# Kernel optimization log

Hardware: AMD Instinct MI355X
Metric: run time of the kernel (lower is better)

The kernel has to match this reference:

```python
import jax, jax.numpy as jnp
import numpy as np

B, S, D = 2, 2048, 1024
H = 16
HD = D // H  # 64


def setup_inputs() -> dict:
    key = jax.random.key(0)
    k1, k2, k3, k4, k5, k6 = jax.random.split(key, 6)
    hidden_states = jax.random.normal(k1, (B, S, D), dtype=jnp.float32)
    attention_mask = jax.random.randint(k2, (B, S), 0, 2, dtype=jnp.int32)
    scale = 1.0 / np.sqrt(D)
    Wq = jax.random.normal(k3, (D, D), dtype=jnp.float32) * scale
    bq = jax.random.normal(k4, (D,), dtype=jnp.float32) * 0.02
    Wk = jax.random.normal(k5, (D, D), dtype=jnp.float32) * scale
    bk = jax.random.normal(k6, (D,), dtype=jnp.float32) * 0.02
    return {"hidden_states": hidden_states, "attention_mask": attention_mask,
            "Wq": Wq, "bq": bq, "Wk": Wk, "bk": bk}


def _split_heads(x):
    # [B, S, D] -> [B, H, S, HD]
    b, s, _ = x.shape
    return x.reshape(b, s, H, HD).transpose(0, 2, 1, 3)


def reference(hidden_states, attention_mask, Wq, bq, Wk, bk):
    dh = jnp.sqrt(jnp.float32(HD))
    q = _split_heads(hidden_states @ Wq + bq)            # [B,H,S,HD]
    k = _split_heads(hidden_states @ Wk + bk)            # [B,H,S,HD]
    v = q + k                                            # value = Q + K
    k_t = -jax.nn.log_sigmoid(-k)                        # negate the logsigmoid(-K) transform
    scores = jnp.einsum('bhqd,bhkd->bhqk', q, k_t) / dh  # [B,H,S,S]
    # mask applied on the QUERY axis (dim 2), broadcast over key axis (faithful to source)
    mask = (attention_mask[:, None, :, None] == 0)       # [B,1,S,1]
    scores = jnp.where(mask, jnp.float32(-10000.0), scores)
    probs = jax.nn.softmax(scores, axis=-1)              # dropout: eval mode (identity)
    ctx = jnp.einsum('bhqk,bhkd->bhqd', probs, v)        # [B,H,S,HD]
    ctx = ctx.transpose(0, 2, 1, 3).reshape(B, S, D)
    return ctx
```

## Files before the change

### kernel.cpp

```cpp
#include <hip/hip_runtime.h>
#include <hip/hip_bf16.h>

#define B_ 2
#define S_ 2048
#define D_ 1024
#define H_ 16
#define HD_ 64

typedef __attribute__((ext_vector_type(8))) short short8;
typedef __attribute__((ext_vector_type(4))) short short4v;
typedef __attribute__((ext_vector_type(4))) float float4v;

typedef const __attribute__((address_space(1))) void* gas_ptr;
typedef __attribute__((address_space(3))) void* las_ptr;

static __device__ inline void gl_lds16(const void* g, void* l) {
  __builtin_amdgcn_global_load_lds((gas_ptr)g, (las_ptr)l, 16, 0, 0);
}

static __device__ inline float b2f(__hip_bfloat16 h) { return __bfloat162float(h); }

static __device__ inline short f2bs(float x) {
  __hip_bfloat16 h = __float2bfloat16(x);
  union { __hip_bfloat16 h; short s; } u; u.h = h; return u.s;
}
static __device__ inline float bs2f(short s) {
  union { short s; __hip_bfloat16 h; } u; u.s = s; return __bfloat162float(u.h);
}
static __device__ inline short4v pk4(float a, float b, float c, float d) {
  union { __hip_bfloat162 h[2]; short4v s; } u;
  u.h[0] = __float22bfloat162_rn(float2{a, b});
  u.h[1] = __float22bfloat162_rn(float2{c, d});
  return u.s;
}

static __device__ inline float4v mfma32(short8 a, short8 b, float4v c) {
  return __builtin_amdgcn_mfma_f32_16x16x32_bf16(a, b, c, 0, 0, 0);
}
static __device__ inline float4v mfma16(short4v a, short4v b, float4v c) {
  return __builtin_amdgcn_mfma_f32_16x16x16bf16_1k(a, b, c, 0, 0, 0);
}

__global__ __launch_bounds__(256) void pre(
    const float* __restrict__ Wq, const float* __restrict__ Wk,
    const float* __restrict__ hs,
    __hip_bfloat16* __restrict__ Wqt, __hip_bfloat16* __restrict__ Wkt,
    __hip_bfloat16* __restrict__ hsb) {
  if (blockIdx.z == 2) {
    const int blk = blockIdx.y * 16 + blockIdx.x;
    for (int it = 0; it < 8; ++it) {
      const size_t i = (size_t)blk * 16384 + it * 2048 + threadIdx.x * 8;
      const float4v v0 = *(const float4v*)(hs + i);
      const float4v v1 = *(const float4v*)(hs + i + 4);
      short8 s;
      for (int j = 0; j < 4; ++j) { s[j] = f2bs(v0[j]); s[4 + j] = f2bs(v1[j]); }
      *(short8*)(hsb + i) = s;
    }
    return;
  }
  const float* W = blockIdx.z ? Wk : Wq;
  __hip_bfloat16* Wt = blockIdx.z ? Wkt : Wqt;
  __shared__ float t[64][65];
  const int n0 = blockIdx.x * 64, k0 = blockIdx.y * 64;
  const int c = threadIdx.x & 63, r0 = threadIdx.x >> 6;
  for (int i = 0; i < 16; ++i) {
    const int r = i * 4 + r0;
    t[c][r] = W[(size_t)(k0 + r) * D_ + n0 + c];
  }
  __syncthreads();
  for (int i = 0; i < 16; ++i) {
    const int rr = i * 4 + r0;
    Wt[(size_t)(n0 + rr) * D_ + k0 + c] = __float2bfloat16(t[rr][c]);
  }
}

__global__ __launch_bounds__(256) void gemm_fused(
    const __hip_bfloat16* __restrict__ A,
    const __hip_bfloat16* __restrict__ Wqt, const __hip_bfloat16* __restrict__ Wkt,
    const float* __restrict__ bq, const float* __restrict__ bk,
    __hip_bfloat16* __restrict__ q_out, __hip_bfloat16* __restrict__ kt_out,
    __hip_bfloat16* __restrict__ vT) {
  const int n0 = blockIdx.x * 128, m0 = blockIdx.y * 64;
  __shared__ __hip_bfloat16 As[2][64 * 32];
  __shared__ __hip_bfloat16 Bq[2][128 * 32];
  __shared__ __hip_bfloat16 Bk[2][128 * 32];
  const int tid = threadIdx.x, wid = tid >> 6, lane = tid & 63;
  const int wm = (wid >> 1) * 32, wn = (wid & 1) * 64;
  const int l15 = lane & 15, l4 = lane >> 4;
  const float4v zz = {0.f, 0.f, 0.f, 0.f};
  float4v accq[2][4], acck[2][4];
  for (int i = 0; i < 2; ++i)
    for (int j = 0; j < 4; ++j) { accq[i][j] = zz; acck[i][j] = zz; }
  const int arow = wid * 16 + (lane >> 2);
  const int brow = wid * 32 + (lane >> 2);
  const int lk8 = (lane & 3) * 8;
  gl_lds16(A + (size_t)(m0 + arow) * D_ + lk8, As[0] + wid * 512);
  gl_lds16(Wqt + (size_t)(n0 + brow) * D_ + lk8, Bq[0] + wid * 1024);
  gl_lds16(Wqt + (size_t)(n0 + brow + 16) * D_ + lk8, Bq[0] + wid * 1024 + 512);
  gl_lds16(Wkt + (size_t)(n0 + brow) * D_ + lk8, Bk[0] + wid * 1024);
  gl_lds16(Wkt + (size_t)(n0 + brow + 16) * D_ + lk8, Bk[0] + wid * 1024 + 512);
  int p = 0;
  for (int kb = 0; kb < 32; ++kb) {
    __syncthreads();
    if (kb < 31) {
      const int kc = (kb + 1) * 32 + lk8;
      gl_lds16(A + (size_t)(m0 + arow) * D_ + kc, As[p ^ 1] + wid * 512);
      gl_lds16(Wqt + (size_t)(n0 + brow) * D_ + kc, Bq[p ^ 1] + wid * 1024);
      gl_lds16(Wqt + (size_t)(n0 + brow + 16) * D_ + kc, Bq[p ^ 1] + wid * 1024 + 512);
      gl_lds16(Wkt + (size_t)(n0 + brow) * D_ + kc, Bk[p ^ 1] + wid * 1024);
      gl_lds16(Wkt + (size_t)(n0 + brow + 16) * D_ + kc, Bk[p ^ 1] + wid * 1024 + 512);
    }
    short8 af[2], bfq[4], bfk[4];
    const int fo = l4 * 8;
    for (int rt = 0; rt < 2; ++rt)
      af[rt] = *(const short8*)(As[p] + (wm + rt * 16 + l15) * 32 + fo);
    for (int ct = 0; ct < 4; ++ct) {
      bfq[ct] = *(const short8*)(Bq[p] + (wn + ct * 16 + l15) * 32 + fo);
      bfk[ct] = *(const short8*)(Bk[p] + (wn + ct * 16 + l15) * 32 + fo);
    }
    for (int rt = 0; rt < 2; ++rt)
      for (int ct = 0; ct < 4; ++ct) {
        accq[rt][ct] = mfma32(af[rt], bfq[ct], accq[rt][ct]);
        acck[rt][ct] = mfma32(af[rt], bfk[ct], acck[rt][ct]);
      }
    p ^= 1;
  }
  float bvq[4], bvk[4];
  for (int ct = 0; ct < 4; ++ct) {
    bvq[ct] = bq[n0 + wn + ct * 16 + l15];
    bvk[ct] = bk[n0 + wn + ct * 16 + l15];
  }
  for (int rt = 0; rt < 2; ++rt)
    for (int ct = 0; ct < 4; ++ct) {
      const int col = n0 + wn + ct * 16 + l15;
      const int h = col >> 6, d = col & 63;
      const int rowb = m0 + wm + rt * 16 + l4 * 4;
      short4v vv;
      for (int r = 0; r < 4; ++r) {
        const int row = rowb + r;
        const float qv = accq[rt][ct][r] + bvq[ct];
        const float kv = acck[rt][ct][r] + bvk[ct];
        const float sp = fmaxf(kv, 0.f) + __logf(1.f + __expf(-fabsf(kv)));
        q_out[(size_t)row * D_ + col] = __float2bfloat16(qv);
        kt_out[(size_t)row * D_ + col] = __float2bfloat16(sp);
        vv[r] = f2bs(qv + kv);
      }
      const int b = rowb >> 11, s = rowb & 2047;
      *(short4v*)(vT + ((size_t)(b * H_ + h) * HD_ + d) * S_ + s) = vv;
    }
}

#define KP 72
__global__ __launch_bounds__(512, 8) void attn(
    const __hip_bfloat16* __restrict__ qb, const __hip_bfloat16* __restrict__ ktb,
    const __hip_bfloat16* __restrict__ vT, const int* __restrict__ mask,
    float* __restrict__ out) {
  __shared__ __hip_bfloat16 smem[2][2 * 64 * KP];
  const int q0 = blockIdx.x * 128, h = blockIdx.y, b = blockIdx.z;
  const int tid = threadIdx.x, wid = tid >> 6, lane = tid & 63;
  const int l15 = lane & 15, l4 = lane >> 4;
  const __hip_bfloat16* qh = qb + (size_t)b * S_ * D_ + h * HD_;
  const __hip_bfloat16* kh = ktb + (size_t)b * S_ * D_ + h * HD_;
  const __hip_bfloat16* vh = vT + (size_t)(b * H_ + h) * HD_ * S_;
  const int voff = 64 * KP;
  const int srow = tid >> 3;
  const int scol = (tid & 7) * 8;

  const int ql = wid * 16 + l15;
  const int qr = q0 + ql;
  const float SC = 0.125f * 1.44269504f;
  const float mq = (mask[b * S_ + qr] != 0) ? SC : 0.f;
  const short8 rq0 = *(const short8*)(qh + (size_t)qr * D_ + l4 * 8);
  const short8 rq1 = *(const short8*)(qh + (size_t)qr * D_ + 32 + l4 * 8);
  short8 bq0, bq1;
  for (int j = 0; j < 8; ++j) {
    bq0[j] = f2bs(bs2f(rq0[j]) * mq);
    bq1[j] = f2bs(bs2f(rq1[j]) * mq);
  }

  const float4v zz = {0.f, 0.f, 0.f, 0.f};
  float4v oacc[4] = {zz, zz, zz, zz};
  float lsum = 0.f;

  short8 gk = *(const short8*)(kh + (size_t)srow * D_ + scol);
  short8 gv = *(const short8*)(vh + (size_t)srow * S_ + scol);

  int p = 0;
  for (int c = 0; c < 32; ++c) {
    *(short8*)&smem[p][srow * KP + scol] = gk;
    *(short8*)&smem[p][voff + srow * KP + scol] = gv;
    __syncthreads();
    if (c < 31) {
      const int kb = (c + 1) * 64;
      gk = *(const short8*)(kh + (size_t)(kb + srow) * D_ + scol);
      gv = *(const short8*)(vh + (size_t)srow * S_ + kb + scol);
    }
    const __hip_bfloat16* kb_ = &smem[p][0];
    const __hip_bfloat16* vb_ = &smem[p][voff];
#pragma unroll
    for (int t = 0; t < 4; ++t) {
      const short8 ak0 = *(const short8*)&kb_[(t * 16 + l15) * KP + l4 * 8];
      const short8 ak1 = *(const short8*)&kb_[(t * 16 + l15) * KP + 32 + l4 * 8];
      float4v cc = zz;
      cc = mfma32(ak0, bq0, cc);
      cc = mfma32(ak1, bq1, cc);
      float e[4];
#pragma unroll
      for (int r = 0; r < 4; ++r) { e[r] = __builtin_amdgcn_exp2f(cc[r]); lsum += e[r]; }
      const short4v pf = pk4(e[0], e[1], e[2], e[3]);
#pragma unroll
      for (int dt = 0; dt < 4; ++dt) {
        const short4v av = *(const short4v*)&vb_[(dt * 16 + l15) * KP + t * 16 + l4 * 4];
        oacc[dt] = mfma16(av, pf, oacc[dt]);
      }
    }
    p ^= 1;
  }
  float l = lsum + __shfl_xor(lsum, 16); l += __shfl_xor(l, 32);
  __syncthreads();
  float* mbuf = (float*)&smem[0][0];
  float* mlb = (float*)&smem[0][0] + 128 * 68;
  #pragma unroll
  for (int dt = 0; dt < 4; ++dt)
#pragma unroll
    for (int r = 0; r < 4; ++r)
      mbuf[ql * 68 + dt * 16 + l4 * 4 + r] = oacc[dt][r];
  if (l4 == 0) mlb[ql] = l;
  __syncthreads();
  const int qq = wid * 16 + (lane >> 2);
  const int dg = (lane & 3) * 16;
  const float li = 1.f / mlb[qq];
  float* orow = out + (size_t)(b * S_ + q0 + qq) * D_ + h * HD_ + dg;
#pragma unroll
  for (int i = 0; i < 4; ++i) {
    float4v v = *(const float4v*)&mbuf[qq * 68 + dg + i * 4];
#pragma unroll
    for (int r = 0; r < 4; ++r) v[r] *= li;
    *(float4v*)(orow + i * 4) = v;
  }
}

extern "C" void kernel_launch(void* const* d_in, const int* in_sizes, int n_in,
                              void* d_out, int out_size, void* d_ws, size_t ws_size,
                              hipStream_t stream) {
  const float* hs = (const float*)d_in[0];
  const int* mask = (const int*)d_in[1];
  const float* Wq = (const float*)d_in[2];
  const float* bq = (const float*)d_in[3];
  const float* Wk = (const float*)d_in[4];
  const float* bk = (const float*)d_in[5];
  float* out = (float*)d_out;
  char* ws = (char*)d_ws;
  const size_t MB = 1u << 20;
  __hip_bfloat16* q_b = (__hip_bfloat16*)(ws + 0 * MB);
  __hip_bfloat16* k_b = (__hip_bfloat16*)(ws + 8 * MB);
  __hip_bfloat16* hsb = (__hip_bfloat16*)(ws + 16 * MB);
  __hip_bfloat16* vT  = (__hip_bfloat16*)(ws + 24 * MB);
  __hip_bfloat16* Wqt = (__hip_bfloat16*)(ws + 32 * MB);
  __hip_bfloat16* Wkt = (__hip_bfloat16*)(ws + 34 * MB);

  pre<<<dim3(16, 16, 3), 256, 0, stream>>>(Wq, Wk, hs, Wqt, Wkt, hsb);
  gemm_fused<<<dim3(8, 64), 256, 0, stream>>>(hsb, Wqt, Wkt, bq, bk, q_b, k_b, vT);
  attn<<<dim3(16, 16, 2), 512, 0, stream>>>(q_b, k_b, vT, mask, out);
}
```

Before: 176.0 us.

## Enlarge GEMM tile, swizzle attention LDS layout, remap attention grid for XCD locality

The fused QK projection GEMM now runs 512 threads on 128x128 tiles, so each loaded weight tile is reused across more rows. The attention kernel drops padded LDS rows in favour of an XOR-swizzled layout, and V is written pre-permuted so each lane reads its P·V operands with wide short8 loads. Attention blocks shrink to 64 queries and 256 threads, and a 1D grid maps each (batch, head) pair to one XCD for L2 locality. P·V MFMAs are now batched after all four score tiles, which raises register pressure and makes correctness depend on the swizzle matching between producer and consumer.

```diff
diff --git a/kernel.cpp b/kernel.cpp
--- a/kernel.cpp
+++ b/kernel.cpp
@@ -74,14 +74,14 @@
   }
 }
 
-__global__ __launch_bounds__(256) void gemm_fused(
+__global__ __launch_bounds__(512, 2) void gemm_fused(
     const __hip_bfloat16* __restrict__ A,
     const __hip_bfloat16* __restrict__ Wqt, const __hip_bfloat16* __restrict__ Wkt,
     const float* __restrict__ bq, const float* __restrict__ bk,
     __hip_bfloat16* __restrict__ q_out, __hip_bfloat16* __restrict__ kt_out,
     __hip_bfloat16* __restrict__ vT) {
-  const int n0 = blockIdx.x * 128, m0 = blockIdx.y * 64;
-  __shared__ __hip_bfloat16 As[2][64 * 32];
+  const int n0 = blockIdx.x * 128, m0 = blockIdx.y * 128;
+  __shared__ __hip_bfloat16 As[2][128 * 32];
   __shared__ __hip_bfloat16 Bq[2][128 * 32];
   __shared__ __hip_bfloat16 Bk[2][128 * 32];
   const int tid = threadIdx.x, wid = tid >> 6, lane = tid & 63;
@@ -91,24 +91,19 @@
   float4v accq[2][4], acck[2][4];
   for (int i = 0; i < 2; ++i)
     for (int j = 0; j < 4; ++j) { accq[i][j] = zz; acck[i][j] = zz; }
-  const int arow = wid * 16 + (lane >> 2);
-  const int brow = wid * 32 + (lane >> 2);
+  const int lrow = wid * 16 + (lane >> 2);
   const int lk8 = (lane & 3) * 8;
-  gl_lds16(A + (size_t)(m0 + arow) * D_ + lk8, As[0] + wid * 512);
-  gl_lds16(Wqt + (size_t)(n0 + brow) * D_ + lk8, Bq[0] + wid * 1024);
-  gl_lds16(Wqt + (size_t)(n0 + brow + 16) * D_ + lk8, Bq[0] + wid * 1024 + 512);
-  gl_lds16(Wkt + (size_t)(n0 + brow) * D_ + lk8, Bk[0] + wid * 1024);
-  gl_lds16(Wkt + (size_t)(n0 + brow + 16) * D_ + lk8, Bk[0] + wid * 1024 + 512);
+  gl_lds16(A + (size_t)(m0 + lrow) * D_ + lk8, As[0] + wid * 512);
+  gl_lds16(Wqt + (size_t)(n0 + lrow) * D_ + lk8, Bq[0] + wid * 512);
+  gl_lds16(Wkt + (size_t)(n0 + lrow) * D_ + lk8, Bk[0] + wid * 512);
   int p = 0;
   for (int kb = 0; kb < 32; ++kb) {
     __syncthreads();
     if (kb < 31) {
       const int kc = (kb + 1) * 32 + lk8;
-      gl_lds16(A + (size_t)(m0 + arow) * D_ + kc, As[p ^ 1] + wid * 512);
-      gl_lds16(Wqt + (size_t)(n0 + brow) * D_ + kc, Bq[p ^ 1] + wid * 1024);
-      gl_lds16(Wqt + (size_t)(n0 + brow + 16) * D_ + kc, Bq[p ^ 1] + wid * 1024 + 512);
-      gl_lds16(Wkt + (size_t)(n0 + brow) * D_ + kc, Bk[p ^ 1] + wid * 1024);
-      gl_lds16(Wkt + (size_t)(n0 + brow + 16) * D_ + kc, Bk[p ^ 1] + wid * 1024 + 512);
+      gl_lds16(A + (size_t)(m0 + lrow) * D_ + kc, As[p ^ 1] + wid * 512);
+      gl_lds16(Wqt + (size_t)(n0 + lrow) * D_ + kc, Bq[p ^ 1] + wid * 512);
+      gl_lds16(Wkt + (size_t)(n0 + lrow) * D_ + kc, Bk[p ^ 1] + wid * 512);
     }
     short8 af[2], bfq[4], bfk[4];
     const int fo = l4 * 8;
@@ -146,25 +141,31 @@
         vv[r] = f2bs(qv + kv);
       }
       const int b = rowb >> 11, s = rowb & 2047;
-      *(short4v*)(vT + ((size_t)(b * H_ + h) * HD_ + d) * S_ + s) = vv;
-    }
-}
-
-#define KP 72
-__global__ __launch_bounds__(512, 8) void attn(
+      const int sw = (s & ~63) | (((s >> 4) & 3) << 2) | (((s >> 2) & 3) << 4);
+      *(short4v*)(vT + ((size_t)(b * H_ + h) * HD_ + d) * S_ + sw) = vv;
+    }
+}
+
+__global__ __launch_bounds__(256, 4) void attn(
     const __hip_bfloat16* __restrict__ qb, const __hip_bfloat16* __restrict__ ktb,
     const __hip_bfloat16* __restrict__ vT, const int* __restrict__ mask,
     float* __restrict__ out) {
-  __shared__ __hip_bfloat16 smem[2][2 * 64 * KP];
-  const int q0 = blockIdx.x * 128, h = blockIdx.y, b = blockIdx.z;
+  __shared__ short smem[16384];
+  const int id = blockIdx.x;
+  const int xcd = id & 7;
+  const int q0 = ((id >> 3) & 31) * 64;
+  const int hb = (id >> 8) * 8 + xcd;
+  const int h = hb >> 1, b = hb & 1;
   const int tid = threadIdx.x, wid = tid >> 6, lane = tid & 63;
   const int l15 = lane & 15, l4 = lane >> 4;
   const __hip_bfloat16* qh = qb + (size_t)b * S_ * D_ + h * HD_;
   const __hip_bfloat16* kh = ktb + (size_t)b * S_ * D_ + h * HD_;
   const __hip_bfloat16* vh = vT + (size_t)(b * H_ + h) * HD_ * S_;
-  const int voff = 64 * KP;
-  const int srow = tid >> 3;
-  const int scol = (tid & 7) * 8;
+  const int srow = tid >> 2;
+  const int b0 = tid & 3;
+  const int sh = srow & 7;
+  const int w0 = srow * 64 + ((b0 ^ sh) * 8);
+  const int w1 = srow * 64 + (((b0 + 4) ^ sh) * 8);
 
   const int ql = wid * 16 + l15;
   const int qr = q0 + ql;
@@ -178,57 +179,78 @@
     bq1[j] = f2bs(bs2f(rq1[j]) * mq);
   }
 
+  const int lsh = l15 & 7;
+  const int ak0off = l15 * 64 + ((l4 ^ lsh) * 8);
+  const int ak1off = l15 * 64 + (((l4 + 4) ^ lsh) * 8);
+  const int vb0off = 4096 + ((2 * l4) ^ lsh) * 8;
+  const int vb1off = 4096 + ((2 * l4 + 1) ^ lsh) * 8;
+
   const float4v zz = {0.f, 0.f, 0.f, 0.f};
   float4v oacc[4] = {zz, zz, zz, zz};
   float lsum = 0.f;
 
-  short8 gk = *(const short8*)(kh + (size_t)srow * D_ + scol);
-  short8 gv = *(const short8*)(vh + (size_t)srow * S_ + scol);
+  short8 gk0 = *(const short8*)(kh + (size_t)srow * D_ + b0 * 8);
+  short8 gk1 = *(const short8*)(kh + (size_t)srow * D_ + b0 * 8 + 32);
+  short8 gv0 = *(const short8*)(vh + (size_t)srow * S_ + b0 * 8);
+  short8 gv1 = *(const short8*)(vh + (size_t)srow * S_ + b0 * 8 + 32);
 
   int p = 0;
   for (int c = 0; c < 32; ++c) {
-    *(short8*)&smem[p][srow * KP + scol] = gk;
-    *(short8*)&smem[p][voff + srow * KP + scol] = gv;
+    short* bufp = smem + p * 8192;
+    *(short8*)(bufp + w0) = gk0;
+    *(short8*)(bufp + w1) = gk1;
+    *(short8*)(bufp + 4096 + w0) = gv0;
+    *(short8*)(bufp + 4096 + w1) = gv1;
     __syncthreads();
     if (c < 31) {
       const int kb = (c + 1) * 64;
-      gk = *(const short8*)(kh + (size_t)(kb + srow) * D_ + scol);
-      gv = *(const short8*)(vh + (size_t)srow * S_ + kb + scol);
-    }
-    const __hip_bfloat16* kb_ = &smem[p][0];
-    const __hip_bfloat16* vb_ = &smem[p][voff];
+      gk0 = *(const short8*)(kh + (size_t)(kb + srow) * D_ + b0 * 8);
+      gk1 = *(const short8*)(kh + (size_t)(kb + srow) * D_ + b0 * 8 + 32);
+      gv0 = *(const short8*)(vh + (size_t)srow * S_ + kb + b0 * 8);
+      gv1 = *(const short8*)(vh + (size_t)srow * S_ + kb + b0 * 8 + 32);
+    }
+    short4v pf[4];
 #pragma unroll
     for (int t = 0; t < 4; ++t) {
-      const short8 ak0 = *(const short8*)&kb_[(t * 16 + l15) * KP + l4 * 8];
-      const short8 ak1 = *(const short8*)&kb_[(t * 16 + l15) * KP + 32 + l4 * 8];
+      const short8 ak0 = *(const short8*)(bufp + t * 1024 + ak0off);
+      const short8 ak1 = *(const short8*)(bufp + t * 1024 + ak1off);
       float4v cc = zz;
       cc = mfma32(ak0, bq0, cc);
       cc = mfma32(ak1, bq1, cc);
       float e[4];
 #pragma unroll
       for (int r = 0; r < 4; ++r) { e[r] = __builtin_amdgcn_exp2f(cc[r]); lsum += e[r]; }
-      const short4v pf = pk4(e[0], e[1], e[2], e[3]);
-#pragma unroll
-      for (int dt = 0; dt < 4; ++dt) {
-        const short4v av = *(const short4v*)&vb_[(dt * 16 + l15) * KP + t * 16 + l4 * 4];
-        oacc[dt] = mfma16(av, pf, oacc[dt]);
-      }
+      pf[t] = pk4(e[0], e[1], e[2], e[3]);
+    }
+#pragma unroll
+    for (int dt = 0; dt < 4; ++dt) {
+      const int rb = (dt * 16 + l15) * 64;
+      const short8 av0 = *(const short8*)(bufp + rb + vb0off);
+      const short8 av1 = *(const short8*)(bufp + rb + vb1off);
+      const short4v a0 = {av0[0], av0[1], av0[2], av0[3]};
+      const short4v a1 = {av0[4], av0[5], av0[6], av0[7]};
+      const short4v a2 = {av1[0], av1[1], av1[2], av1[3]};
+      const short4v a3 = {av1[4], av1[5], av1[6], av1[7]};
+      oacc[dt] = mfma16(a0, pf[0], oacc[dt]);
+      oacc[dt] = mfma16(a1, pf[1], oacc[dt]);
+      oacc[dt] = mfma16(a2, pf[2], oacc[dt]);
+      oacc[dt] = mfma16(a3, pf[3], oacc[dt]);
     }
     p ^= 1;
   }
   float l = lsum + __shfl_xor(lsum, 16); l += __shfl_xor(l, 32);
   __syncthreads();
-  float* mbuf = (float*)&smem[0][0];
-  float* mlb = (float*)&smem[0][0] + 128 * 68;
-  #pragma unroll
+  float* mbuf = (float*)smem;
+  float* mlb = (float*)smem + 64 * 68;
+#pragma unroll
   for (int dt = 0; dt < 4; ++dt)
 #pragma unroll
     for (int r = 0; r < 4; ++r)
       mbuf[ql * 68 + dt * 16 + l4 * 4 + r] = oacc[dt][r];
   if (l4 == 0) mlb[ql] = l;
   __syncthreads();
-  const int qq = wid * 16 + (lane >> 2);
-  const int dg = (lane & 3) * 16;
+  const int qq = tid >> 2;
+  const int dg = (tid & 3) * 16;
   const float li = 1.f / mlb[qq];
   float* orow = out + (size_t)(b * S_ + q0 + qq) * D_ + h * HD_ + dg;
 #pragma unroll
@@ -260,6 +282,6 @@
   __hip_bfloat16* Wkt = (__hip_bfloat16*)(ws + 34 * MB);
 
   pre<<<dim3(16, 16, 3), 256, 0, stream>>>(Wq, Wk, hs, Wqt, Wkt, hsb);
-  gemm_fused<<<dim3(8, 64), 256, 0, stream>>>(hsb, Wqt, Wkt, bq, bk, q_b, k_b, vT);
-  attn<<<dim3(16, 16, 2), 512, 0, stream>>>(q_b, k_b, vT, mask, out);
-}
+  gemm_fused<<<dim3(8, 32), 512, 0, stream>>>(hsb, Wqt, Wkt, bq, bk, q_b, k_b, vT);
+  attn<<<dim3(1024), 256, 0, stream>>>(q_b, k_b, vT, mask, out);
+}
```

Result: faster. 165.9 us (-5.7%).
